# Kernel optimization log

Measured on AMD Instinct MI355X. Metric: run time of the kernel, lower is better.

Reference implementation:

```python
import jax, jax.numpy as jnp
import numpy as np

NUM_HOP = 3
VOCAB = 32000
D = 512          # embed_dim
MEM = 60         # memory_size (> story_size -> T_A slice branch)
BS = 64
STORY = 50
SENT = 32        # max_sent_size
QLEN = 16


def positional_encoding(J, d):
    # pe[i-1, k-1] = 1 - i/J - (k/d) * (1 - 2*i/J), i in 1..J, k in 1..d
    i = jnp.arange(1, J + 1, dtype=jnp.float32)[:, None]
    k = jnp.arange(1, d + 1, dtype=jnp.float32)[None, :]
    return 1.0 - i / J - (k / d) * (1.0 - 2.0 * i / J)


def setup_inputs() -> dict:
    key = jax.random.key(0)
    kA, kT, kC, kQ = jax.random.split(key, 4)
    # stacked embedding tables A[0..num_hop], each (VOCAB, D), N(0, 0.1)
    A = jax.random.normal(kA, (NUM_HOP + 1, VOCAB, D), dtype=jnp.float32) * 0.1
    T_A = jax.random.normal(kT, (1, MEM, D), dtype=jnp.float32) * 0.1
    context = jax.random.randint(kC, (BS, STORY, SENT), 0, VOCAB)
    query = jax.random.randint(kQ, (BS, QLEN), 0, VOCAB)
    return {"context": context, "query": query, "A": A, "T_A": T_A}


def reference(context, query, A, T_A):
    # padding_idx=0: row 0 of every table is zero
    A = A.at[:, 0, :].set(0.0)
    pe = positional_encoding(SENT, D)              # (SENT, D)

    # query encoding: u = B(query).sum(axis=1), B = A[0]; dropout is identity at eval
    u = A[0][query].sum(axis=1)                    # (BS, D)

    for h in range(NUM_HOP):
        # memory embedding with positional encoding, summed over words
        m = (A[h][context] * pe).sum(axis=2)       # (BS, STORY, D)
        # temporal encoding: memory_size > story_size branch
        m = m + T_A[:, :STORY, :]
        # output embedding (no positional encoding applied in original)
        c = A[h + 1][context].sum(axis=2)          # (BS, STORY, D)
        p = jax.nn.softmax(jnp.einsum('bsd,bd->bs', m, u), axis=1)
        u = u + jnp.einsum('bs,bsd->bd', p, c)

    # W = A[-1].weight.T -> logits = u @ W
    logits = u @ A[NUM_HOP].T                      # (BS, VOCAB)
    return jax.nn.softmax(logits, axis=-1)
```

## Files before the change

### kernel.cpp

```cpp
#include <hip/hip_runtime.h>
#include <math.h>

#define NUM_HOP 3
#define VOCAB   32000
#define DIM     512
#define MEM     60
#define BS      64
#define STORY   50
#define SENT    32
#define QLEN    16

#define TBL     ((size_t)VOCAB * DIM)

typedef _Float16 v8h __attribute__((ext_vector_type(8)));
typedef float    v4f __attribute__((ext_vector_type(4)));

static __device__ __forceinline__ ushort f2h(float x) {
    union { _Float16 h; ushort u; } v;
    v.h = (_Float16)x;
    return v.u;
}

__global__ __launch_bounds__(512) void k_prep(const float* __restrict__ A0,
                                              const int*   __restrict__ query,
                                              float*       __restrict__ u) {
    const int b = blockIdx.x, tid = threadIdx.x;
    const int* q = query + b * QLEN;
    int idx[QLEN];
    #pragma unroll
    for (int t = 0; t < QLEN; ++t) idx[t] = q[t];
    float acc = 0.f;
    #pragma unroll
    for (int t = 0; t < QLEN; ++t)
        if (idx[t] != 0) acc += A0[(size_t)idx[t] * DIM + tid];
    u[(size_t)b * DIM + tid] = acc;
}

__global__ __launch_bounds__(256) void k_z(const float* __restrict__ Ah,
                                           const float* __restrict__ T_A,
                                           const float* __restrict__ u,
                                           float*       __restrict__ Z) {
    __shared__ ushort Ahl[32 * 128];
    __shared__ ushort Uhl[128 * 128];
    const int tid  = threadIdx.x;
    const int lane = tid & 63;
    const int wave = tid >> 6;
    const int i16  = lane & 15;
    const int quad = lane >> 4;
    const int mt   = wave & 1;
    const int nh   = wave >> 1;
    const bool ist = (blockIdx.x >= 1000);
    const int row0 = blockIdx.x * 32;

    v4f acc[4];
    #pragma unroll
    for (int nt = 0; nt < 4; ++nt) acc[nt] = (v4f){0.f, 0.f, 0.f, 0.f};

    for (int ko = 0; ko < 4; ++ko) {
        __syncthreads();
        #pragma unroll
        for (int it = 0; it < 2; ++it) {
            const int i = it * 256 + tid;
            const int r = i >> 4, g = i & 15;
            const float* src;
            if (ist) {
                int t = row0 + r - VOCAB; if (t > MEM - 1) t = MEM - 1;
                src = T_A + (size_t)t * DIM + ko * 128 + g * 8;
            } else {
                src = Ah + (size_t)(row0 + r) * DIM + ko * 128 + g * 8;
            }
            const float4 f0 = *(const float4*)(src);
            const float4 f1 = *(const float4*)(src + 4);
            union { ushort h[8]; uint4 q; } pk;
            pk.h[0] = f2h(f0.x); pk.h[1] = f2h(f0.y);
            pk.h[2] = f2h(f0.z); pk.h[3] = f2h(f0.w);
            pk.h[4] = f2h(f1.x); pk.h[5] = f2h(f1.y);
            pk.h[6] = f2h(f1.z); pk.h[7] = f2h(f1.w);
            *(uint4*)(&Ahl[r * 128 + ((g ^ (r & 7)) * 8)]) = pk.q;
        }
        #pragma unroll
        for (int it = 0; it < 8; ++it) {
            const int i = it * 256 + tid;
            const int n = i >> 4, g = i & 15;
            const int k = ko * 128 + g * 8;
            const float* su = u + (size_t)(n & 63) * DIM + k;
            union { float f[8]; float4 v[2]; } ld;
            ld.v[0] = *(const float4*)(su);
            ld.v[1] = *(const float4*)(su + 4);
            if (n >= 64) {
                #pragma unroll
                for (int j = 0; j < 8; ++j)
                    ld.f[j] *= (float)(k + j + 1) * (1.0f / (float)DIM);
            }
            union { ushort h[8]; uint4 q; } pk;
            #pragma unroll
            for (int j = 0; j < 8; ++j) pk.h[j] = f2h(ld.f[j]);
            *(uint4*)(&Uhl[n * 128 + ((g ^ (n & 7)) * 8)]) = pk.q;
        }
        __syncthreads();

        const int ar = mt * 16 + i16;
        #pragma unroll
        for (int ki = 0; ki < 4; ++ki) {
            const int ga = ki * 4 + quad;
            const v8h a = *(const v8h*)(&Ahl[ar * 128 + ((ga ^ (ar & 7)) * 8)]);
            #pragma unroll
            for (int nt = 0; nt < 4; ++nt) {
                const int n = nh * 64 + nt * 16 + i16;
                const v8h bb = *(const v8h*)(&Uhl[n * 128 + ((ga ^ (n & 7)) * 8)]);
                acc[nt] = __builtin_amdgcn_mfma_f32_16x16x32_f16(a, bb, acc[nt], 0, 0, 0);
            }
        }
    }

    const int vb = row0 + mt * 16 + quad * 4;
    #pragma unroll
    for (int nt = 0; nt < 4; ++nt) {
        const int col = nh * 64 + nt * 16 + i16;
        #pragma unroll
        for (int r = 0; r < 4; ++r)
            Z[(size_t)(vb + r) * 128 + col] = acc[nt][r];
    }
}

__global__ __launch_bounds__(256) void k_score(const int*   __restrict__ ctx,
                                               const float* __restrict__ Z,
                                               float*       __restrict__ p) {
    const int b    = blockIdx.x;
    const int tid  = threadIdx.x;
    const int wave = tid >> 6;
    const int lane = tid & 63;
    const int w    = lane & 31;
    const int half = lane >> 5;
    __shared__ float ss[64];

    const float aw = 1.0f - (float)(w + 1) * (1.0f / 32.0f);
    const float bw = 1.0f - (float)(w + 1) * (1.0f / 16.0f);

    #pragma unroll
    for (int i = 0; i < 7; ++i) {
        const int s = i * 8 + wave * 2 + half;
        float val = 0.f;
        if (s < STORY) {
            const int idx = ctx[b * (STORY * SENT) + s * SENT + w];
            if (idx != 0) {
                const float zu = Z[(size_t)idx * 128 + b];
                const float zd = Z[(size_t)idx * 128 + 64 + b];
                val = aw * zu - bw * zd;
            }
        }
        val += __shfl_down(val, 16); val += __shfl_down(val, 8);
        val += __shfl_down(val, 4);  val += __shfl_down(val, 2);
        val += __shfl_down(val, 1);
        if (w == 0 && s < STORY)
            ss[s] = val + Z[(size_t)(VOCAB + s) * 128 + b];
    }
    __syncthreads();

    if (tid < 64) {
        const float v = (tid < STORY) ? ss[tid] : -1e30f;
        float mx = v;
        for (int off = 32; off; off >>= 1) mx = fmaxf(mx, __shfl_down(mx, off));
        mx = __shfl(mx, 0);
        const float e = (tid < STORY) ? __expf(v - mx) : 0.f;
        float sm = e;
        for (int off = 32; off; off >>= 1) sm += __shfl_down(sm, off);
        sm = __shfl(sm, 0);
        p[b * 64 + tid] = e / sm;
    }
}

__global__ __launch_bounds__(512) void k_cupd(const int*   __restrict__ ctx,
                                              const float* __restrict__ p,
                                              const float* __restrict__ An,
                                              float*       __restrict__ u) {
    const int b    = blockIdx.x >> 2;
    const int q    = blockIdx.x & 3;
    const int tid  = threadIdx.x;
    const int wave = tid >> 6;
    const int lane = tid & 63;
    const int d0   = lane * 8;
    __shared__ float ps[64];
    __shared__ float red[8][DIM];

    if (tid < 64) ps[tid] = p[b * 64 + tid];
    __syncthreads();

    const int* cb = ctx + b * (STORY * SENT);
    float acc[8];
    #pragma unroll
    for (int j = 0; j < 8; ++j) acc[j] = 0.f;

    const int base = q * 400 + wave * 50;
    #pragma unroll 5
    for (int i = 0; i < 50; ++i) {
        const int t = base + i;
        const int idx = cb[t];
        const float pw = (idx != 0) ? ps[t >> 5] : 0.f;
        const float* row = An + (size_t)idx * DIM + d0;
        const float4 r0 = *(const float4*)(row);
        const float4 r1 = *(const float4*)(row + 4);
        acc[0] = fmaf(pw, r0.x, acc[0]); acc[1] = fmaf(pw, r0.y, acc[1]);
        acc[2] = fmaf(pw, r0.z, acc[2]); acc[3] = fmaf(pw, r0.w, acc[3]);
        acc[4] = fmaf(pw, r1.x, acc[4]); acc[5] = fmaf(pw, r1.y, acc[5]);
        acc[6] = fmaf(pw, r1.z, acc[6]); acc[7] = fmaf(pw, r1.w, acc[7]);
    }
    #pragma unroll
    for (int j = 0; j < 8; ++j) red[wave][d0 + j] = acc[j];
    __syncthreads();

    float s = 0.f;
    #pragma unroll
    for (int wv = 0; wv < 8; ++wv) s += red[wv][tid];
    atomicAdd(&u[(size_t)b * DIM + tid], s);
}

#define DCH 64
__global__ __launch_bounds__(256) void k_logits(const float* __restrict__ A3,
                                                const float* __restrict__ u,
                                                float*       __restrict__ out) {
    __shared__ float AT[DCH][64];
    __shared__ float UT[DCH][64];
    const int tid = threadIdx.x;
    const int v0  = blockIdx.x * 64;
    const int vq  = (tid & 15) * 4;
    const int bq  = (tid >> 4) * 4;
    const int lr  = tid & 63;
    const int dg  = tid >> 6;

    float4 acc[4];
    #pragma unroll
    for (int j = 0; j < 4; ++j) acc[j] = make_float4(0.f, 0.f, 0.f, 0.f);

    for (int ko = 0; ko < 8; ++ko) {
        __syncthreads();
        #pragma unroll
        for (int k4 = 0; k4 < 4; ++k4) {
            const int dd = dg * 16 + k4 * 4;
            const float4 a = *(const float4*)(A3 + (size_t)(v0 + lr) * DIM + ko * DCH + dd);
            AT[dd + 0][lr] = a.x; AT[dd + 1][lr] = a.y;
            AT[dd + 2][lr] = a.z; AT[dd + 3][lr] = a.w;
            const float4 b = *(const float4*)(u + (size_t)lr * DIM + ko * DCH + dd);
            UT[dd + 0][lr] = b.x; UT[dd + 1][lr] = b.y;
            UT[dd + 2][lr] = b.z; UT[dd + 3][lr] = b.w;
        }
        __syncthreads();
        #pragma unroll 4
        for (int dd = 0; dd < DCH; ++dd) {
            const float4 a4 = *(const float4*)(&AT[dd][vq]);
            const float4 u4 = *(const float4*)(&UT[dd][bq]);
            acc[0].x = fmaf(a4.x, u4.x, acc[0].x); acc[0].y = fmaf(a4.y, u4.x, acc[0].y);
            acc[0].z = fmaf(a4.z, u4.x, acc[0].z); acc[0].w = fmaf(a4.w, u4.x, acc[0].w);
            acc[1].x = fmaf(a4.x, u4.y, acc[1].x); acc[1].y = fmaf(a4.y, u4.y, acc[1].y);
            acc[1].z = fmaf(a4.z, u4.y, acc[1].z); acc[1].w = fmaf(a4.w, u4.y, acc[1].w);
            acc[2].x = fmaf(a4.x, u4.z, acc[2].x); acc[2].y = fmaf(a4.y, u4.z, acc[2].y);
            acc[2].z = fmaf(a4.z, u4.z, acc[2].z); acc[2].w = fmaf(a4.w, u4.z, acc[2].w);
            acc[3].x = fmaf(a4.x, u4.w, acc[3].x); acc[3].y = fmaf(a4.y, u4.w, acc[3].y);
            acc[3].z = fmaf(a4.z, u4.w, acc[3].z); acc[3].w = fmaf(a4.w, u4.w, acc[3].w);
        }
    }

    if (v0 + vq == 0) {
        acc[0].x = 0.f; acc[1].x = 0.f; acc[2].x = 0.f; acc[3].x = 0.f;
    }
    #pragma unroll
    for (int j = 0; j < 4; ++j)
        *(float4*)(out + (size_t)(bq + j) * VOCAB + v0 + vq) = acc[j];
}

__global__ __launch_bounds__(1024) void k_vsm(float* __restrict__ out) {
    const int b   = blockIdx.x;
    const int tid = threadIdx.x;
    float* row = out + (size_t)b * VOCAB;
    __shared__ float red[16];
    __shared__ float bc;

    float x[32];
    #pragma unroll
    for (int k = 0; k < 31; ++k) x[k] = row[tid + k * 1024];
    const bool extra = (tid < VOCAB - 31 * 1024);
    x[31] = extra ? row[tid + 31 * 1024] : -1e30f;

    float mx = -1e30f;
    #pragma unroll
    for (int k = 0; k < 32; ++k) mx = fmaxf(mx, x[k]);
    for (int off = 32; off; off >>= 1) mx = fmaxf(mx, __shfl_down(mx, off));
    if ((tid & 63) == 0) red[tid >> 6] = mx;
    __syncthreads();
    if (tid < 64) {
        float v = (tid < 16) ? red[tid] : -1e30f;
        for (int off = 8; off; off >>= 1) v = fmaxf(v, __shfl_down(v, off));
        if (tid == 0) bc = v;
    }
    __syncthreads();
    mx = bc;
    __syncthreads();

    float sum = 0.f;
    #pragma unroll
    for (int k = 0; k < 32; ++k) { x[k] = __expf(x[k] - mx); sum += x[k]; }
    if (!extra) sum -= x[31];
    for (int off = 32; off; off >>= 1) sum += __shfl_down(sum, off);
    if ((tid & 63) == 0) red[tid >> 6] = sum;
    __syncthreads();
    if (tid < 64) {
        float v = (tid < 16) ? red[tid] : 0.f;
        for (int off = 8; off; off >>= 1) v += __shfl_down(v, off);
        if (tid == 0) bc = v;
    }
    __syncthreads();
    const float inv = 1.0f / bc;

    #pragma unroll
    for (int k = 0; k < 31; ++k) row[tid + k * 1024] = x[k] * inv;
    if (extra) row[tid + 31 * 1024] = x[31] * inv;
}

extern "C" void kernel_launch(void* const* d_in, const int* in_sizes, int n_in,
                              void* d_out, int out_size, void* d_ws, size_t ws_size,
                              hipStream_t stream) {
    const int*   ctx   = (const int*)d_in[0];
    const int*   query = (const int*)d_in[1];
    const float* A     = (const float*)d_in[2];
    const float* T_A   = (const float*)d_in[3];
    float* out = (float*)d_out;

    float* u = (float*)d_ws;
    float* p = u + BS * DIM;
    float* Z = p + BS * 64;

    k_prep<<<BS, DIM, 0, stream>>>(A, query, u);
    for (int h = 0; h < NUM_HOP; ++h) {
        k_z    <<<1002, 256, 0, stream>>>(A + (size_t)h * TBL, T_A, u, Z);
        k_score<<<BS, 256, 0, stream>>>(ctx, Z, p);
        k_cupd <<<BS * 4, 512, 0, stream>>>(ctx, p, A + (size_t)(h + 1) * TBL, u);
    }
    k_logits<<<500, 256, 0, stream>>>(A + 3 * TBL, u, out);
    k_vsm  <<<BS, 1024, 0, stream>>>(out);
}
```

Before: 550.8 us.

## Precompute fp16 query operands and use MFMA for logits GEMM

Result: slower. 592.8 us (+7.6%).

```diff
diff --git a/kernel.cpp b/kernel.cpp
--- a/kernel.cpp
+++ b/kernel.cpp
@@ -23,7 +23,8 @@
 
 __global__ __launch_bounds__(512) void k_prep(const float* __restrict__ A0,
                                               const int*   __restrict__ query,
-                                              float*       __restrict__ u) {
+                                              float*       __restrict__ u,
+                                              ushort*      __restrict__ U2h) {
     const int b = blockIdx.x, tid = threadIdx.x;
     const int* q = query + b * QLEN;
     int idx[QLEN];
@@ -34,86 +35,63 @@
     for (int t = 0; t < QLEN; ++t)
         if (idx[t] != 0) acc += A0[(size_t)idx[t] * DIM + tid];
     u[(size_t)b * DIM + tid] = acc;
-}
-
-__global__ __launch_bounds__(256) void k_z(const float* __restrict__ Ah,
-                                           const float* __restrict__ T_A,
-                                           const float* __restrict__ u,
-                                           float*       __restrict__ Z) {
-    __shared__ ushort Ahl[32 * 128];
-    __shared__ ushort Uhl[128 * 128];
+    U2h[(size_t)b * DIM + tid] = f2h(acc);
+    U2h[(size_t)(BS + b) * DIM + tid] = f2h(acc * (float)(tid + 1) * (1.0f / (float)DIM));
+}
+
+__global__ __launch_bounds__(512) void k_uref(const float* __restrict__ u,
+                                              ushort*      __restrict__ U2h) {
+    const int b = blockIdx.x, tid = threadIdx.x;
+    const float un = u[(size_t)b * DIM + tid];
+    U2h[(size_t)b * DIM + tid] = f2h(un);
+    U2h[(size_t)(BS + b) * DIM + tid] = f2h(un * (float)(tid + 1) * (1.0f / (float)DIM));
+}
+
+__global__ __launch_bounds__(256) void k_z(const float*  __restrict__ Ah,
+                                           const float*  __restrict__ T_A,
+                                           const ushort* __restrict__ U2h,
+                                           float*        __restrict__ Z) {
     const int tid  = threadIdx.x;
     const int lane = tid & 63;
     const int wave = tid >> 6;
     const int i16  = lane & 15;
     const int quad = lane >> 4;
-    const int mt   = wave & 1;
-    const int nh   = wave >> 1;
-    const bool ist = (blockIdx.x >= 1000);
-    const int row0 = blockIdx.x * 32;
+    const int task = blockIdx.x * 4 + wave;
+    const int rt   = task >> 1;
+    const int nh   = task & 1;
+    const int row  = rt * 16 + i16;
+
+    const float* arow;
+    if (row < VOCAB) {
+        arow = Ah + (size_t)row * DIM;
+    } else {
+        int t = row - VOCAB; if (t > MEM - 1) t = MEM - 1;
+        arow = T_A + (size_t)t * DIM;
+    }
+    const ushort* ub = U2h + (size_t)(nh * 64) * DIM;
 
     v4f acc[4];
     #pragma unroll
     for (int nt = 0; nt < 4; ++nt) acc[nt] = (v4f){0.f, 0.f, 0.f, 0.f};
 
-    for (int ko = 0; ko < 4; ++ko) {
-        __syncthreads();
-        #pragma unroll
-        for (int it = 0; it < 2; ++it) {
-            const int i = it * 256 + tid;
-            const int r = i >> 4, g = i & 15;
-            const float* src;
-            if (ist) {
-                int t = row0 + r - VOCAB; if (t > MEM - 1) t = MEM - 1;
-                src = T_A + (size_t)t * DIM + ko * 128 + g * 8;
-            } else {
-                src = Ah + (size_t)(row0 + r) * DIM + ko * 128 + g * 8;
-            }
-            const float4 f0 = *(const float4*)(src);
-            const float4 f1 = *(const float4*)(src + 4);
-            union { ushort h[8]; uint4 q; } pk;
-            pk.h[0] = f2h(f0.x); pk.h[1] = f2h(f0.y);
-            pk.h[2] = f2h(f0.z); pk.h[3] = f2h(f0.w);
-            pk.h[4] = f2h(f1.x); pk.h[5] = f2h(f1.y);
-            pk.h[6] = f2h(f1.z); pk.h[7] = f2h(f1.w);
-            *(uint4*)(&Ahl[r * 128 + ((g ^ (r & 7)) * 8)]) = pk.q;
-        }
-        #pragma unroll
-        for (int it = 0; it < 8; ++it) {
-            const int i = it * 256 + tid;
-            const int n = i >> 4, g = i & 15;
-            const int k = ko * 128 + g * 8;
-            const float* su = u + (size_t)(n & 63) * DIM + k;
-            union { float f[8]; float4 v[2]; } ld;
-            ld.v[0] = *(const float4*)(su);
-            ld.v[1] = *(const float4*)(su + 4);
-            if (n >= 64) {
-                #pragma unroll
-                for (int j = 0; j < 8; ++j)
-                    ld.f[j] *= (float)(k + j + 1) * (1.0f / (float)DIM);
-            }
-            union { ushort h[8]; uint4 q; } pk;
-            #pragma unroll
-            for (int j = 0; j < 8; ++j) pk.h[j] = f2h(ld.f[j]);
-            *(uint4*)(&Uhl[n * 128 + ((g ^ (n & 7)) * 8)]) = pk.q;
-        }
-        __syncthreads();
-
-        const int ar = mt * 16 + i16;
-        #pragma unroll
-        for (int ki = 0; ki < 4; ++ki) {
-            const int ga = ki * 4 + quad;
-            const v8h a = *(const v8h*)(&Ahl[ar * 128 + ((ga ^ (ar & 7)) * 8)]);
-            #pragma unroll
-            for (int nt = 0; nt < 4; ++nt) {
-                const int n = nh * 64 + nt * 16 + i16;
-                const v8h bb = *(const v8h*)(&Uhl[n * 128 + ((ga ^ (n & 7)) * 8)]);
-                acc[nt] = __builtin_amdgcn_mfma_f32_16x16x32_f16(a, bb, acc[nt], 0, 0, 0);
-            }
-        }
-    }
-
-    const int vb = row0 + mt * 16 + quad * 4;
+    #pragma unroll 4
+    for (int ki = 0; ki < 16; ++ki) {
+        const int k0 = ki * 32 + quad * 8;
+        const float4 a0 = *(const float4*)(arow + k0);
+        const float4 a1 = *(const float4*)(arow + k0 + 4);
+        v8h af;
+        af[0] = (_Float16)a0.x; af[1] = (_Float16)a0.y;
+        af[2] = (_Float16)a0.z; af[3] = (_Float16)a0.w;
+        af[4] = (_Float16)a1.x; af[5] = (_Float16)a1.y;
+        af[6] = (_Float16)a1.z; af[7] = (_Float16)a1.w;
+        #pragma unroll
+        for (int nt = 0; nt < 4; ++nt) {
+            const v8h bf = *(const v8h*)(ub + (size_t)(nt * 16 + i16) * DIM + k0);
+            acc[nt] = __builtin_amdgcn_mfma_f32_16x16x32_f16(af, bf, acc[nt], 0, 0, 0);
+        }
+    }
+
+    const int vb = rt * 16 + quad * 4;
     #pragma unroll
     for (int nt = 0; nt < 4; ++nt) {
         const int col = nh * 64 + nt * 16 + i16;
@@ -215,57 +193,73 @@
     atomicAdd(&u[(size_t)b * DIM + tid], s);
 }
 
-#define DCH 64
-__global__ __launch_bounds__(256) void k_logits(const float* __restrict__ A3,
-                                                const float* __restrict__ u,
-                                                float*       __restrict__ out) {
-    __shared__ float AT[DCH][64];
-    __shared__ float UT[DCH][64];
-    const int tid = threadIdx.x;
-    const int v0  = blockIdx.x * 64;
-    const int vq  = (tid & 15) * 4;
-    const int bq  = (tid >> 4) * 4;
-    const int lr  = tid & 63;
-    const int dg  = tid >> 6;
-
-    float4 acc[4];
-    #pragma unroll
-    for (int j = 0; j < 4; ++j) acc[j] = make_float4(0.f, 0.f, 0.f, 0.f);
-
-    for (int ko = 0; ko < 8; ++ko) {
+__global__ __launch_bounds__(256) void k_logits(const float*  __restrict__ A3,
+                                                const ushort* __restrict__ U2h,
+                                                float*        __restrict__ out) {
+    __shared__ ushort Abf[64 * 128];
+    __shared__ ushort Ubf[64 * 128];
+    const int tid  = threadIdx.x;
+    const int lane = tid & 63;
+    const int wave = tid >> 6;
+    const int i16  = lane & 15;
+    const int quad = lane >> 4;
+    const int row0 = blockIdx.x * 64;
+
+    v4f acc[4];
+    #pragma unroll
+    for (int nt = 0; nt < 4; ++nt) acc[nt] = (v4f){0.f, 0.f, 0.f, 0.f};
+
+    for (int ko = 0; ko < 4; ++ko) {
         __syncthreads();
         #pragma unroll
-        for (int k4 = 0; k4 < 4; ++k4) {
-            const int dd = dg * 16 + k4 * 4;
-            const float4 a = *(const float4*)(A3 + (size_t)(v0 + lr) * DIM + ko * DCH + dd);
-            AT[dd + 0][lr] = a.x; AT[dd + 1][lr] = a.y;
-            AT[dd + 2][lr] = a.z; AT[dd + 3][lr] = a.w;
-            const float4 b = *(const float4*)(u + (size_t)lr * DIM + ko * DCH + dd);
-            UT[dd + 0][lr] = b.x; UT[dd + 1][lr] = b.y;
-            UT[dd + 2][lr] = b.z; UT[dd + 3][lr] = b.w;
+        for (int it = 0; it < 4; ++it) {
+            const int i = it * 256 + tid;
+            const int r = i >> 4, g = i & 15;
+            const float* src = A3 + ((size_t)(row0 + r)) * DIM + ko * 128 + g * 8;
+            const float4 f0 = *(const float4*)(src);
+            const float4 f1 = *(const float4*)(src + 4);
+            union { ushort h[8]; uint4 q; } pk;
+            pk.h[0] = f2h(f0.x); pk.h[1] = f2h(f0.y);
+            pk.h[2] = f2h(f0.z); pk.h[3] = f2h(f0.w);
+            pk.h[4] = f2h(f1.x); pk.h[5] = f2h(f1.y);
+            pk.h[6] = f2h(f1.z); pk.h[7] = f2h(f1.w);
+            *(uint4*)(&Abf[r * 128 + ((g ^ (r & 7)) * 8)]) = pk.q;
+        }
+        #pragma unroll
+        for (int it = 0; it < 4; ++it) {
+            const int i = it * 256 + tid;
+            const int n = i >> 4, g = i & 15;
+            const uint4 v = *(const uint4*)(U2h + (size_t)n * DIM + ko * 128 + g * 8);
+            *(uint4*)(&Ubf[n * 128 + ((g ^ (n & 7)) * 8)]) = v;
         }
         __syncthreads();
-        #pragma unroll 4
-        for (int dd = 0; dd < DCH; ++dd) {
-            const float4 a4 = *(const float4*)(&AT[dd][vq]);
-            const float4 u4 = *(const float4*)(&UT[dd][bq]);
-            acc[0].x = fmaf(a4.x, u4.x, acc[0].x); acc[0].y = fmaf(a4.y, u4.x, acc[0].y);
-            acc[0].z = fmaf(a4.z, u4.x, acc[0].z); acc[0].w = fmaf(a4.w, u4.x, acc[0].w);
-            acc[1].x = fmaf(a4.x, u4.y, acc[1].x); acc[1].y = fmaf(a4.y, u4.y, acc[1].y);
-            acc[1].z = fmaf(a4.z, u4.y, acc[1].z); acc[1].w = fmaf(a4.w, u4.y, acc[1].w);
-            acc[2].x = fmaf(a4.x, u4.z, acc[2].x); acc[2].y = fmaf(a4.y, u4.z, acc[2].y);
-            acc[2].z = fmaf(a4.z, u4.z, acc[2].z); acc[2].w = fmaf(a4.w, u4.z, acc[2].w);
-            acc[3].x = fmaf(a4.x, u4.w, acc[3].x); acc[3].y = fmaf(a4.y, u4.w, acc[3].y);
-            acc[3].z = fmaf(a4.z, u4.w, acc[3].z); acc[3].w = fmaf(a4.w, u4.w, acc[3].w);
-        }
-    }
-
-    if (v0 + vq == 0) {
-        acc[0].x = 0.f; acc[1].x = 0.f; acc[2].x = 0.f; acc[3].x = 0.f;
-    }
-    #pragma unroll
-    for (int j = 0; j < 4; ++j)
-        *(float4*)(out + (size_t)(bq + j) * VOCAB + v0 + vq) = acc[j];
+
+        const int arow = wave * 16 + i16;
+        #pragma unroll
+        for (int ki = 0; ki < 4; ++ki) {
+            const int ga = ki * 4 + quad;
+            const v8h a = *(const v8h*)(&Abf[arow * 128 + ((ga ^ (arow & 7)) * 8)]);
+            #pragma unroll
+            for (int nt = 0; nt < 4; ++nt) {
+                const int n = nt * 16 + i16;
+                const v8h bb = *(const v8h*)(&Ubf[n * 128 + ((ga ^ (n & 7)) * 8)]);
+                acc[nt] = __builtin_amdgcn_mfma_f32_16x16x32_f16(a, bb, acc[nt], 0, 0, 0);
+            }
+        }
+    }
+
+    const int vbase = row0 + wave * 16 + quad * 4;
+    if (vbase == 0) {
+        #pragma unroll
+        for (int nt = 0; nt < 4; ++nt) acc[nt][0] = 0.f;
+    }
+    #pragma unroll
+    for (int nt = 0; nt < 4; ++nt) {
+        const int bcol = nt * 16 + i16;
+        #pragma unroll
+        for (int r = 0; r < 4; ++r)
+            out[(size_t)bcol * VOCAB + vbase + r] = acc[nt][r];
+    }
 }
 
 __global__ __launch_bounds__(1024) void k_vsm(float* __restrict__ out) {
@@ -325,16 +319,18 @@
     const float* T_A   = (const float*)d_in[3];
     float* out = (float*)d_out;
 
-    float* u = (float*)d_ws;
-    float* p = u + BS * DIM;
-    float* Z = p + BS * 64;
-
-    k_prep<<<BS, DIM, 0, stream>>>(A, query, u);
+    float*  u   = (float*)d_ws;
+    ushort* U2h = (ushort*)(u + BS * DIM);
+    float*  p   = (float*)(U2h + 2 * BS * DIM);
+    float*  Z   = p + BS * 64;
+
+    k_prep<<<BS, DIM, 0, stream>>>(A, query, u, U2h);
     for (int h = 0; h < NUM_HOP; ++h) {
-        k_z    <<<1002, 256, 0, stream>>>(A + (size_t)h * TBL, T_A, u, Z);
+        k_z    <<<1002, 256, 0, stream>>>(A + (size_t)h * TBL, T_A, U2h, Z);
         k_score<<<BS, 256, 0, stream>>>(ctx, Z, p);
         k_cupd <<<BS * 4, 512, 0, stream>>>(ctx, p, A + (size_t)(h + 1) * TBL, u);
-    }
-    k_logits<<<500, 256, 0, stream>>>(A + 3 * TBL, u, out);
+        k_uref <<<BS, 512, 0, stream>>>(u, U2h);
+    }
+    k_logits<<<500, 256, 0, stream>>>(A + 3 * TBL, U2h, out);
     k_vsm  <<<BS, 1024, 0, stream>>>(out);
 }
```
